# Optimization experiments

Measured on AMD Instinct MI355X. Metric: run time of the kernel, lower is better.

Reference implementation:

```python
import jax, jax.numpy as jnp
import numpy as np

HEADS = 4
DIM_HEAD = 32
GROUPS = 32  # min(256//4, 32)
EPS = 1e-5


def setup_inputs() -> dict:
    key = jax.random.key(0)
    ks = jax.random.split(key, 5)
    B, C, H, W = 16, 256, 64, 64
    CD, HC, WC = 512, 32, 32
    hid = HEADS * DIM_HEAD  # 128
    return {
        "x": jax.random.normal(ks[0], (B, C, H, W), jnp.float32),
        "cond": jax.random.normal(ks[1], (B, CD, HC, WC), jnp.float32),
        "gn_w": jnp.ones((C,), jnp.float32),
        "gn_b": jnp.zeros((C,), jnp.float32),
        "w_q": jax.random.normal(ks[2], (hid, C), jnp.float32) * 0.05,
        "b_q": jnp.zeros((hid,), jnp.float32),
        "w_kv": jax.random.normal(ks[3], (2 * hid, CD), jnp.float32) * 0.05,
        "b_kv": jnp.zeros((2 * hid,), jnp.float32),
        "w_out": jax.random.normal(ks[4], (C, hid), jnp.float32) * 0.05,
        "b_out": jnp.zeros((C,), jnp.float32),
    }


def _group_norm(x, w, b):
    # x: (B, C, H, W); normalize per group over (channels-in-group, H, W)
    B, C, H, W = x.shape
    xg = x.reshape(B, GROUPS, C // GROUPS, H, W)
    mu = jnp.mean(xg, axis=(2, 3, 4), keepdims=True)
    var = jnp.var(xg, axis=(2, 3, 4), keepdims=True)
    xn = ((xg - mu) * jax.lax.rsqrt(var + EPS)).reshape(B, C, H, W)
    return xn * w[None, :, None, None] + b[None, :, None, None]


def _conv1x1(x, w, b):
    # x: (B, Cin, H, W), w: (Cout, Cin), b: (Cout,)
    return jnp.einsum('oc,bchw->bohw', w, x) + b[None, :, None, None]


def reference(x, cond, gn_w, gn_b, w_q, b_q, w_kv, b_kv, w_out, b_out):
    B, C, H, W = x.shape
    hid = HEADS * DIM_HEAD
    xn = _group_norm(x, gn_w, gn_b)
    q = _conv1x1(xn, w_q, b_q)          # (B, hid, H, W)
    kv = _conv1x1(cond, w_kv, b_kv)     # (B, 2*hid, Hc, Wc)
    Nc = kv.shape[2] * kv.shape[3]
    N = H * W
    k = kv[:, :hid].reshape(B, HEADS, DIM_HEAD, Nc)
    v = kv[:, hid:].reshape(B, HEADS, DIM_HEAD, Nc)
    q = q.reshape(B, HEADS, DIM_HEAD, N)
    k = jax.nn.softmax(k, axis=-1)
    # kv outer product: (B, heads, d, e)
    context = jnp.einsum('bhdn,bhen->bhde', k, v)
    # query contraction over d: (B, heads, e, n)
    out = jnp.einsum('bhde,bhdn->bhen', context, q)
    out = out.reshape(B, hid, H, W)
    return _conv1x1(out, w_out, b_out)
```

## Files before the change

### kernel.cpp

```cpp
#include <hip/hip_runtime.h>
#include <hip/hip_bf16.h>

typedef __attribute__((ext_vector_type(8))) short bf16x8;
typedef __attribute__((ext_vector_type(4))) float f32x4;

__device__ __forceinline__ ushort f2bf(float f) {
    __hip_bfloat16 h = __float2bfloat16(f);
    return __builtin_bit_cast(ushort, h);
}
__device__ __forceinline__ unsigned pack2(float a, float b) {
    return (unsigned)f2bf(a) | ((unsigned)f2bf(b) << 16);
}
__device__ __forceinline__ float bflo(unsigned u) { return __uint_as_float(u << 16); }
__device__ __forceinline__ float bfhi(unsigned u) { return __uint_as_float(u & 0xffff0000u); }

__device__ __forceinline__ void unpack8(uint4 r, float* o) {
    o[0] = bflo(r.x); o[1] = bfhi(r.x); o[2] = bflo(r.y); o[3] = bfhi(r.y);
    o[4] = bflo(r.z); o[5] = bfhi(r.z); o[6] = bflo(r.w); o[7] = bfhi(r.w);
}

__global__ __launch_bounds__(256) void kv_gemm(const float* __restrict__ w_kv,
                                               const float* __restrict__ cond,
                                               const float* __restrict__ b_kv,
                                               ushort* __restrict__ kv16,
                                               float* __restrict__ zbase) {
    __shared__ ushort lA[128 * 64];
    __shared__ ushort lB[32 * 64];
    __shared__ float scratch[64 * 32];
    int nc = blockIdx.x, rb = blockIdx.y, b = blockIdx.z;
    int t = threadIdx.x;
    int fid = blockIdx.x + 32 * (blockIdx.y + 2 * blockIdx.z);
    if (fid < 264) zbase[fid * 256 + t] = 0.f;
    int col0 = nc * 32, row0 = rb * 128;
    int l = t & 63, w = t >> 6;
    int lr = l & 15, lg = l >> 4;
    const float* Ab32 = w_kv + (size_t)row0 * 512;
    const float* Bb = cond + (size_t)b * 512 * 1024 + col0;
    int rA = t >> 3, gAr = t & 7, gw = gAr ^ (rA & 7);
    int rB = t >> 3, gB = t & 7;
    int sp = t & 31, sj4 = (t >> 5) & 7;
    float4 ka0_, ka1_, ka2_, ka3_, ka4_, ka5_, ka6_, ka7_;
    float4 kb0_, kb1_;
#define KG_LOADA(k0) { \
    ka0_ = *(const float4*)&Ab32[(size_t)(rA)      * 512 + (k0) + gAr * 8]; \
    ka1_ = *(const float4*)&Ab32[(size_t)(rA)      * 512 + (k0) + gAr * 8 + 4]; \
    ka2_ = *(const float4*)&Ab32[(size_t)(32 + rA) * 512 + (k0) + gAr * 8]; \
    ka3_ = *(const float4*)&Ab32[(size_t)(32 + rA) * 512 + (k0) + gAr * 8 + 4]; \
    ka4_ = *(const float4*)&Ab32[(size_t)(64 + rA) * 512 + (k0) + gAr * 8]; \
    ka5_ = *(const float4*)&Ab32[(size_t)(64 + rA) * 512 + (k0) + gAr * 8 + 4]; \
    ka6_ = *(const float4*)&Ab32[(size_t)(96 + rA) * 512 + (k0) + gAr * 8]; \
    ka7_ = *(const float4*)&Ab32[(size_t)(96 + rA) * 512 + (k0) + gAr * 8 + 4]; }
#define KG_LOADB(k0) { \
    kb0_ = *(const float4*)&Bb[(size_t)((k0) + rB)      * 1024 + gB * 4]; \
    kb1_ = *(const float4*)&Bb[(size_t)((k0) + 32 + rB) * 1024 + gB * 4]; }
#define KG_WRITEA() { uint4 p; \
    p.x = pack2(ka0_.x, ka0_.y); p.y = pack2(ka0_.z, ka0_.w); \
    p.z = pack2(ka1_.x, ka1_.y); p.w = pack2(ka1_.z, ka1_.w); \
    *(uint4*)((char*)lA + (size_t)((rA)      * 8 + gw) * 16) = p; \
    p.x = pack2(ka2_.x, ka2_.y); p.y = pack2(ka2_.z, ka2_.w); \
    p.z = pack2(ka3_.x, ka3_.y); p.w = pack2(ka3_.z, ka3_.w); \
    *(uint4*)((char*)lA + (size_t)((32 + rA) * 8 + gw) * 16) = p; \
    p.x = pack2(ka4_.x, ka4_.y); p.y = pack2(ka4_.z, ka4_.w); \
    p.z = pack2(ka5_.x, ka5_.y); p.w = pack2(ka5_.z, ka5_.w); \
    *(uint4*)((char*)lA + (size_t)((64 + rA) * 8 + gw) * 16) = p; \
    p.x = pack2(ka6_.x, ka6_.y); p.y = pack2(ka6_.z, ka6_.w); \
    p.z = pack2(ka7_.x, ka7_.y); p.w = pack2(ka7_.z, ka7_.w); \
    *(uint4*)((char*)lA + (size_t)((96 + rA) * 8 + gw) * 16) = p; }
#define KG_WRITEB() { \
    *(float4*)((char*)scratch + (rB)      * 128 + ((gB ^ (((rB)      >> 1) & 7)) * 16)) = kb0_; \
    *(float4*)((char*)scratch + (32 + rB) * 128 + ((gB ^ (((32 + rB) >> 1) & 7)) * 16)) = kb1_; }
#define KG_PACKB() { \
    int js = sj4 ^ (sp & 7); \
    float4 s0 = *(const float4*)((char*)scratch + (2*sp)   * 128 + js * 16); \
    float4 s2 = *(const float4*)((char*)scratch + (2*sp+1) * 128 + js * 16); \
    float c0v[4] = {s0.x, s0.y, s0.z, s0.w}; \
    float c1v[4] = {s2.x, s2.y, s2.z, s2.w}; \
    _Pragma("unroll") \
    for (int w4 = 0; w4 < 4; ++w4) { \
        int n = sj4 * 4 + w4; \
        unsigned pk = pack2(c0v[w4], c1v[w4]); \
        *(unsigned*)((char*)lB + n * 128 + (((sp >> 2) ^ (n & 7)) * 16) + (sp & 3) * 4) = pk; \
    } }
    KG_LOADA(0); KG_LOADB(0);
    f32x4 acc[2][2] = {};
    for (int it = 0; it < 8; ++it) {
        KG_WRITEA();
        KG_WRITEB();
        __syncthreads();
        if (it < 7) { KG_LOADA(it * 64 + 64); KG_LOADB(it * 64 + 64); }
        KG_PACKB();
        __syncthreads();
        __builtin_amdgcn_s_setprio(1);
        #pragma unroll
        for (int ks = 0; ks < 2; ++ks) {
            bf16x8 av[2], bv[2];
            #pragma unroll
            for (int mi = 0; mi < 2; ++mi) {
                int ar = w * 32 + mi * 16 + lr;
                int q = (ks * 4 + lg) ^ (ar & 7);
                av[mi] = *(const bf16x8*)((const char*)lA + ar * 128 + q * 16);
            }
            #pragma unroll
            for (int ni = 0; ni < 2; ++ni) {
                int br = ni * 16 + lr;
                int q = (ks * 4 + lg) ^ (br & 7);
                bv[ni] = *(const bf16x8*)((const char*)lB + br * 128 + q * 16);
            }
            #pragma unroll
            for (int mi = 0; mi < 2; ++mi)
                #pragma unroll
                for (int ni = 0; ni < 2; ++ni)
                    acc[mi][ni] = __builtin_amdgcn_mfma_f32_16x16x32_bf16(
                        av[mi], bv[ni], acc[mi][ni], 0, 0, 0);
        }
        __builtin_amdgcn_s_setprio(0);
        __syncthreads();
    }
#undef KG_LOADA
#undef KG_LOADB
#undef KG_WRITEA
#undef KG_WRITEB
#undef KG_PACKB
    int orow = row0 + w * 32;
    #pragma unroll
    for (int mi = 0; mi < 2; ++mi) {
        int rbase = orow + mi * 16 + lg * 4;
        float4 b4 = *(const float4*)&b_kv[rbase];
        float bvr[4] = {b4.x, b4.y, b4.z, b4.w};
        #pragma unroll
        for (int ni = 0; ni < 2; ++ni) {
            int cc = col0 + ni * 16 + lr;
            #pragma unroll
            for (int r = 0; r < 4; ++r)
                kv16[((size_t)b * 256 + rbase + r) * 1024 + cc] = f2bf(acc[mi][ni][r] + bvr[r]);
        }
    }
}

__global__ __launch_bounds__(256) void ctxstats_kernel(const ushort* __restrict__ kv,
                                                       const float* __restrict__ x,
                                                       float* __restrict__ rowsum,
                                                       float* __restrict__ ctx,
                                                       float* __restrict__ statacc) {
    __shared__ float pl[32][129], vl[32][129];
    int bid = blockIdx.x, t = threadIdx.x;
    if (bid < 512) {
        int bh = bid >> 3, b = bh >> 2, h = bh & 3;
        int n0 = (bid & 7) * 128;
        int r = t >> 3, cs = (t & 7) * 16;
        const ushort* kp = kv + ((size_t)b * 256 + h * 32 + r) * 1024 + n0 + cs;
        const ushort* vp = kv + ((size_t)b * 256 + 128 + h * 32 + r) * 1024 + n0 + cs;
        float kvals[16], vvals[16];
        unpack8(((const uint4*)kp)[0], kvals);
        unpack8(((const uint4*)kp)[1], kvals + 8);
        unpack8(((const uint4*)vp)[0], vvals);
        unpack8(((const uint4*)vp)[1], vvals + 8);
        float psum = 0.f;
        #pragma unroll
        for (int i = 0; i < 16; ++i) {
            float e = __expf(kvals[i]);
            pl[r][cs + i] = e;
            vl[r][cs + i] = vvals[i];
            psum += e;
        }
        psum += __shfl_xor(psum, 1, 64);
        psum += __shfl_xor(psum, 2, 64);
        psum += __shfl_xor(psum, 4, 64);
        if ((t & 7) == 0) atomicAdd(&rowsum[bh * 32 + r], psum);
        __syncthreads();
        int d0 = t >> 5, e0 = t & 31;
        float acc[4] = {0.f, 0.f, 0.f, 0.f};
        #pragma unroll 8
        for (int nn = 0; nn < 128; ++nn) {
            float vv = vl[e0][nn];
            #pragma unroll
            for (int i = 0; i < 4; ++i)
                acc[i] += pl[d0 + 8 * i][nn] * vv;
        }
        #pragma unroll
        for (int i = 0; i < 4; ++i)
            atomicAdd(&ctx[((size_t)bh * 32 + d0 + 8 * i) * 32 + e0], acc[i]);
    } else {
        int bg = bid - 512;
        const float4* xp = (const float4*)(x + (size_t)bg * 32768);
        float s = 0.f, ss = 0.f;
        #pragma unroll
        for (int j = 0; j < 32; ++j) {
            float4 v = xp[t + 256 * j];
            s  += v.x + v.y + v.z + v.w;
            ss += v.x*v.x + v.y*v.y + v.z*v.z + v.w*v.w;
        }
        #pragma unroll
        for (int off = 32; off > 0; off >>= 1) {
            s  += __shfl_down(s, off, 64);
            ss += __shfl_down(ss, off, 64);
        }
        int wave = t >> 6;
        if ((t & 63) == 0) { pl[0][wave * 2] = s; pl[0][wave * 2 + 1] = ss; }
        __syncthreads();
        if (t == 0) {
            statacc[bg * 2]     = pl[0][0] + pl[0][2] + pl[0][4] + pl[0][6];
            statacc[bg * 2 + 1] = pl[0][1] + pl[0][3] + pl[0][5] + pl[0][7];
        }
    }
}

__global__ __launch_bounds__(256) void a_kernel(const float* __restrict__ ctx,
                                                const float* __restrict__ rowsum,
                                                const float* __restrict__ w_out,
                                                const float* __restrict__ w_q,
                                                const float* __restrict__ b_q,
                                                const float* __restrict__ b_out,
                                                ushort* __restrict__ A16,
                                                float* __restrict__ biasb) {
    __shared__ float ctxl[4][32][33];
    __shared__ float wol[16][128];
    __shared__ float ml[16][128];
    int b = blockIdx.x >> 4, ot = (blockIdx.x & 15) << 4;
    int t = threadIdx.x;
    #pragma unroll
    for (int j = 0; j < 16; ++j) {
        int e = t + 256 * j;
        float inv = 1.f / rowsum[b * 128 + (e >> 5)];
        ctxl[e >> 10][(e >> 5) & 31][e & 31] = ctx[(size_t)b * 4096 + e] * inv;
    }
    #pragma unroll
    for (int j = 0; j < 8; ++j) {
        int e = t + 256 * j;
        wol[e >> 7][e & 127] = w_out[(ot + (e >> 7)) * 128 + (e & 127)];
    }
    __syncthreads();
    #pragma unroll
    for (int j = 0; j < 8; ++j) {
        int e = t + 256 * j;
        int o = e >> 7, hd = e & 127, h = hd >> 5, d = hd & 31;
        float acc = 0.f;
        #pragma unroll
        for (int ee = 0; ee < 32; ++ee) acc += wol[o][h * 32 + ee] * ctxl[h][d][ee];
        ml[o][hd] = acc;
    }
    __syncthreads();
    int c = t;
    float wt[16];
    #pragma unroll
    for (int o = 0; o < 16; ++o) wt[o] = 0.f;
    for (int hd = 0; hd < 128; ++hd) {
        float wq = w_q[hd * 256 + c];
        #pragma unroll
        for (int o = 0; o < 16; ++o) wt[o] += ml[o][hd] * wq;
    }
    ushort* Abp = A16 + ((size_t)b * 256 + ot) * 256 + c;
    #pragma unroll
    for (int o = 0; o < 16; ++o)
        Abp[(size_t)o * 256] = f2bf(wt[o]);
    if (t < 16) {
        int o = t;
        float md = 0.f;
        #pragma unroll 8
        for (int hd = 0; hd < 128; ++hd) md += ml[o][hd] * b_q[hd];
        biasb[(size_t)b * 256 + ot + o] = md + b_out[ot + o];
    }
}

__global__ __launch_bounds__(512) void out_gemm_fused(const ushort* __restrict__ A16,
                                                      const float* __restrict__ x,
                                                      const float* __restrict__ statacc,
                                                      const float* __restrict__ gn_w,
                                                      const float* __restrict__ gn_b,
                                                      const float* __restrict__ biasb,
                                                      float* __restrict__ out) {
    __shared__ ushort lA[256 * 64];
    __shared__ ushort lB[64 * 64];
    __shared__ float scratch[64 * 64];
    __shared__ float sct[256][2];
    int b = blockIdx.y;
    int n0 = blockIdx.x * 64;
    int t = threadIdx.x;
    int l = t & 63, wid = t >> 6;
    int wr = wid >> 1, wc = wid & 1;
    int lr = l & 15, lg = l >> 4;
    const ushort* Ab = A16 + (size_t)b * 65536;
    const float* xb = x + (size_t)b * 256 * 4096 + n0;
    int sp = t & 31, sj4 = t >> 5;
    if (t < 256) {
        int g = t >> 3;
        float S  = statacc[(b * 32 + g) * 2];
        float SS = statacc[(b * 32 + g) * 2 + 1];
        float mu  = S * (1.f / 32768.f);
        float var = SS * (1.f / 32768.f) - mu * mu;
        float sc = rsqrtf(var + 1e-5f) * gn_w[t];
        sct[t][0] = sc;
        sct[t][1] = gn_b[t] - mu * sc;
    }
    uint4 a0_, a1_, a2_, a3_;
    float4 b0_, b1_;
    float4 c0_, c1_;
    int rA = t >> 3, gA = (t & 7) ^ (rA & 7);
    int rB = t >> 4, gB = t & 15;
#define OG_LOADA(k0) { \
    a0_ = *(const uint4*)(Ab + (size_t)(rA)       * 256 + (k0) + gA * 8); \
    a1_ = *(const uint4*)(Ab + (size_t)(64 + rA)  * 256 + (k0) + gA * 8); \
    a2_ = *(const uint4*)(Ab + (size_t)(128 + rA) * 256 + (k0) + gA * 8); \
    a3_ = *(const uint4*)(Ab + (size_t)(192 + rA) * 256 + (k0) + gA * 8); }
#define OG_LOADB0(k0) { \
    b0_ = *(const float4*)&xb[(size_t)((k0) + rB)      * 4096 + gB * 4]; \
    b1_ = *(const float4*)&xb[(size_t)((k0) + 32 + rB) * 4096 + gB * 4]; }
#define OG_LOADB1(k0) { \
    c0_ = *(const float4*)&xb[(size_t)((k0) + rB)      * 4096 + gB * 4]; \
    c1_ = *(const float4*)&xb[(size_t)((k0) + 32 + rB) * 4096 + gB * 4]; }
#define OG_WRITEB(v0, v1) { \
    *(float4*)((char*)scratch + (rB)      * 256 + ((gB ^ (((rB)      >> 1) & 15)) * 16)) = v0; \
    *(float4*)((char*)scratch + (32 + rB) * 256 + ((gB ^ (((32 + rB) >> 1) & 15)) * 16)) = v1; }
    OG_LOADA(0); OG_LOADB0(0); 
    f32x4 acc[4][2] = {};
    for (int it = 0; it < 4; ++it) {
        int k0 = it * 64;
        *(uint4*)((char*)lA + (size_t)t * 16)          = a0_;
        *(uint4*)((char*)lA + (size_t)(512 + t) * 16)  = a1_;
        *(uint4*)((char*)lA + (size_t)(1024 + t) * 16) = a2_;
        *(uint4*)((char*)lA + (size_t)(1536 + t) * 16) = a3_;
        if (it & 1) { OG_WRITEB(c0_, c1_); } else { OG_WRITEB(b0_, b1_); }
        __syncthreads();
        if (it < 3) OG_LOADA(k0 + 64);
        if (it == 0) OG_LOADB1(64);
        if (it == 1 && 1) OG_LOADB0(128);
        if (it == 2) OG_LOADB1(192);
        {
            int js = sj4 ^ (sp & 15);
            float sc0 = sct[k0 + 2 * sp][0],     tc0 = sct[k0 + 2 * sp][1];
            float sc1 = sct[k0 + 2 * sp + 1][0], tc1 = sct[k0 + 2 * sp + 1][1];
            float4 s0 = *(const float4*)((char*)scratch + (2*sp)   * 256 + js * 16);
            float4 s2 = *(const float4*)((char*)scratch + (2*sp+1) * 256 + js * 16);
            float c0v[4] = {s0.x, s0.y, s0.z, s0.w};
            float c1v[4] = {s2.x, s2.y, s2.z, s2.w};
            #pragma unroll
            for (int w4 = 0; w4 < 4; ++w4) {
                int n = sj4 * 4 + w4;
                unsigned pk = pack2(c0v[w4] * sc0 + tc0, c1v[w4] * sc1 + tc1);
                *(unsigned*)((char*)lB + n * 128 + (((sp >> 2) ^ (n & 7)) * 16) + (sp & 3) * 4) = pk;
            }
        }
        __syncthreads();
        __builtin_amdgcn_s_setprio(1);
        #pragma unroll
        for (int ks = 0; ks < 2; ++ks) {
            bf16x8 av[4], bv[2];
            #pragma unroll
            for (int mi = 0; mi < 4; ++mi) {
                int ar = wr * 64 + mi * 16 + lr;
                int q = (ks * 4 + lg) ^ (ar & 7);
                av[mi] = *(const bf16x8*)((const char*)lA + ar * 128 + q * 16);
            }
            #pragma unroll
            for (int ni = 0; ni < 2; ++ni) {
                int br = wc * 32 + ni * 16 + lr;
                int q = (ks * 4 + lg) ^ (br & 7);
                bv[ni] = *(const bf16x8*)((const char*)lB + br * 128 + q * 16);
            }
            #pragma unroll
            for (int mi = 0; mi < 4; ++mi)
                #pragma unroll
                for (int ni = 0; ni < 2; ++ni)
                    acc[mi][ni] = __builtin_amdgcn_mfma_f32_16x16x32_bf16(
                        av[mi], bv[ni], acc[mi][ni], 0, 0, 0);
        }
        __builtin_amdgcn_s_setprio(0);
        __syncthreads();
    }
#undef OG_LOADA
#undef OG_LOADB0
#undef OG_LOADB1
#undef OG_WRITEB
    const float* bp = biasb + (size_t)b * 256;
    int orow = wr * 64, ocol = n0 + wc * 32 + lr;
    #pragma unroll
    for (int mi = 0; mi < 4; ++mi) {
        int rb2 = orow + mi * 16 + lg * 4;
        float4 b4 = *(const float4*)&bp[rb2];
        float bvr[4] = {b4.x, b4.y, b4.z, b4.w};
        #pragma unroll
        for (int ni = 0; ni < 2; ++ni) {
            int cc = ocol + ni * 16;
            #pragma unroll
            for (int r = 0; r < 4; ++r)
                out[((size_t)b * 256 + rb2 + r) * 4096 + cc] = acc[mi][ni][r] + bvr[r];
        }
    }
}

extern "C" void kernel_launch(void* const* d_in, const int* in_sizes, int n_in,
                              void* d_out, int out_size, void* d_ws, size_t ws_size,
                              hipStream_t stream) {
    const float* x     = (const float*)d_in[0];
    const float* cond  = (const float*)d_in[1];
    const float* gn_w  = (const float*)d_in[2];
    const float* gn_b  = (const float*)d_in[3];
    const float* w_q   = (const float*)d_in[4];
    const float* b_q   = (const float*)d_in[5];
    const float* w_kv  = (const float*)d_in[6];
    const float* b_kv  = (const float*)d_in[7];
    const float* w_out = (const float*)d_in[8];
    const float* b_out = (const float*)d_in[9];
    float* out = (float*)d_out;

    float* f       = (float*)d_ws;
    float* statacc = f;
    float* rowsum  = f + 1024;
    float* ctx     = f + 3072;
    float* biasb   = f + 68608;
    ushort* u      = (ushort*)(f + 72704);
    ushort* kv16   = u;
    ushort* A16    = u + 4194304;

    kv_gemm<<<dim3(32, 2, 16), 256, 0, stream>>>(w_kv, cond, b_kv, kv16, rowsum);
    ctxstats_kernel<<<1024, 256, 0, stream>>>(kv16, x, rowsum, ctx, statacc);
    a_kernel<<<256, 256, 0, stream>>>(ctx, rowsum, w_out, w_q, b_q, b_out, A16, biasb);
    out_gemm_fused<<<dim3(64, 16), 512, 0, stream>>>(A16, x, statacc, gn_w, gn_b, biasb, out);
}
```

Before: 78.29 us.

## Fold GroupNorm affine into A16 weights and bias; swizzle block order for XCD locality

```diff
diff --git a/kernel.cpp b/kernel.cpp
--- a/kernel.cpp
+++ b/kernel.cpp
@@ -27,10 +27,12 @@
     __shared__ ushort lA[128 * 64];
     __shared__ ushort lB[32 * 64];
     __shared__ float scratch[64 * 32];
-    int nc = blockIdx.x, rb = blockIdx.y, b = blockIdx.z;
+    int bid0 = blockIdx.x;
+    int swz = (bid0 & 7) * 128 + (bid0 >> 3);
+    int b = swz >> 6, rem = swz & 63;
+    int rb = rem >> 5, nc = rem & 31;
     int t = threadIdx.x;
-    int fid = blockIdx.x + 32 * (blockIdx.y + 2 * blockIdx.z);
-    if (fid < 264) zbase[fid * 256 + t] = 0.f;
+    if (bid0 < 264) zbase[bid0 * 256 + t] = 0.f;
     int col0 = nc * 32, row0 = rb * 128;
     int l = t & 63, w = t >> 6;
     int lr = l & 15, lg = l >> 4;
@@ -210,12 +212,17 @@
                                                 const float* __restrict__ w_out,
                                                 const float* __restrict__ w_q,
                                                 const float* __restrict__ b_q,
+                                                const float* __restrict__ statacc,
+                                                const float* __restrict__ gn_w,
+                                                const float* __restrict__ gn_b,
                                                 const float* __restrict__ b_out,
                                                 ushort* __restrict__ A16,
                                                 float* __restrict__ biasb) {
     __shared__ float ctxl[4][32][33];
     __shared__ float wol[16][128];
     __shared__ float ml[16][128];
+    __shared__ float cbuf[256][17];
+    __shared__ float pbuf[16][17];
     int b = blockIdx.x >> 4, ot = (blockIdx.x & 15) << 4;
     int t = threadIdx.x;
     #pragma unroll
@@ -240,7 +247,12 @@
         ml[o][hd] = acc;
     }
     __syncthreads();
-    int c = t;
+    int c = t, g = c >> 3;
+    float a0 = statacc[(b * 32 + g) * 2], a1 = statacc[(b * 32 + g) * 2 + 1];
+    float mu  = a0 * (1.f / 32768.f);
+    float var = a1 * (1.f / 32768.f) - mu * mu;
+    float sc = rsqrtf(var + 1e-5f) * gn_w[c];
+    float tc = gn_b[c] - mu * sc;
     float wt[16];
     #pragma unroll
     for (int o = 0; o < 16; ++o) wt[o] = 0.f;
@@ -251,30 +263,42 @@
     }
     ushort* Abp = A16 + ((size_t)b * 256 + ot) * 256 + c;
     #pragma unroll
-    for (int o = 0; o < 16; ++o)
-        Abp[(size_t)o * 256] = f2bf(wt[o]);
+    for (int o = 0; o < 16; ++o) {
+        Abp[(size_t)o * 256] = f2bf(wt[o] * sc);
+        cbuf[c][o] = wt[o] * tc;
+    }
+    __syncthreads();
+    {
+        int o = t >> 4, seg = t & 15;
+        float p = 0.f;
+        #pragma unroll
+        for (int i = 0; i < 16; ++i) p += cbuf[seg * 16 + i][o];
+        pbuf[o][seg] = p;
+    }
+    __syncthreads();
     if (t < 16) {
         int o = t;
+        float sum = 0.f;
+        #pragma unroll
+        for (int s2 = 0; s2 < 16; ++s2) sum += pbuf[o][s2];
         float md = 0.f;
         #pragma unroll 8
         for (int hd = 0; hd < 128; ++hd) md += ml[o][hd] * b_q[hd];
-        biasb[(size_t)b * 256 + ot + o] = md + b_out[ot + o];
+        biasb[(size_t)b * 256 + ot + o] = sum + md + b_out[ot + o];
     }
 }
 
 __global__ __launch_bounds__(512) void out_gemm_fused(const ushort* __restrict__ A16,
                                                       const float* __restrict__ x,
-                                                      const float* __restrict__ statacc,
-                                                      const float* __restrict__ gn_w,
-                                                      const float* __restrict__ gn_b,
                                                       const float* __restrict__ biasb,
                                                       float* __restrict__ out) {
     __shared__ ushort lA[256 * 64];
     __shared__ ushort lB[64 * 64];
     __shared__ float scratch[64 * 64];
-    __shared__ float sct[256][2];
-    int b = blockIdx.y;
-    int n0 = blockIdx.x * 64;
+    int bid0 = blockIdx.x;
+    int swz = (bid0 & 7) * 128 + (bid0 >> 3);
+    int b = swz >> 6, nb = swz & 63;
+    int n0 = nb * 64;
     int t = threadIdx.x;
     int l = t & 63, wid = t >> 6;
     int wr = wid >> 1, wc = wid & 1;
@@ -282,16 +306,6 @@
     const ushort* Ab = A16 + (size_t)b * 65536;
     const float* xb = x + (size_t)b * 256 * 4096 + n0;
     int sp = t & 31, sj4 = t >> 5;
-    if (t < 256) {
-        int g = t >> 3;
-        float S  = statacc[(b * 32 + g) * 2];
-        float SS = statacc[(b * 32 + g) * 2 + 1];
-        float mu  = S * (1.f / 32768.f);
-        float var = SS * (1.f / 32768.f) - mu * mu;
-        float sc = rsqrtf(var + 1e-5f) * gn_w[t];
-        sct[t][0] = sc;
-        sct[t][1] = gn_b[t] - mu * sc;
-    }
     uint4 a0_, a1_, a2_, a3_;
     float4 b0_, b1_;
     float4 c0_, c1_;
@@ -311,7 +325,7 @@
 #define OG_WRITEB(v0, v1) { \
     *(float4*)((char*)scratch + (rB)      * 256 + ((gB ^ (((rB)      >> 1) & 15)) * 16)) = v0; \
     *(float4*)((char*)scratch + (32 + rB) * 256 + ((gB ^ (((32 + rB) >> 1) & 15)) * 16)) = v1; }
-    OG_LOADA(0); OG_LOADB0(0); 
+    OG_LOADA(0); OG_LOADB0(0);
     f32x4 acc[4][2] = {};
     for (int it = 0; it < 4; ++it) {
         int k0 = it * 64;
@@ -323,12 +337,10 @@
         __syncthreads();
         if (it < 3) OG_LOADA(k0 + 64);
         if (it == 0) OG_LOADB1(64);
-        if (it == 1 && 1) OG_LOADB0(128);
+        if (it == 1) OG_LOADB0(128);
         if (it == 2) OG_LOADB1(192);
         {
             int js = sj4 ^ (sp & 15);
-            float sc0 = sct[k0 + 2 * sp][0],     tc0 = sct[k0 + 2 * sp][1];
-            float sc1 = sct[k0 + 2 * sp + 1][0], tc1 = sct[k0 + 2 * sp + 1][1];
             float4 s0 = *(const float4*)((char*)scratch + (2*sp)   * 256 + js * 16);
             float4 s2 = *(const float4*)((char*)scratch + (2*sp+1) * 256 + js * 16);
             float c0v[4] = {s0.x, s0.y, s0.z, s0.w};
@@ -336,7 +348,7 @@
             #pragma unroll
             for (int w4 = 0; w4 < 4; ++w4) {
                 int n = sj4 * 4 + w4;
-                unsigned pk = pack2(c0v[w4] * sc0 + tc0, c1v[w4] * sc1 + tc1);
+                unsigned pk = pack2(c0v[w4], c1v[w4]);
                 *(unsigned*)((char*)lB + n * 128 + (((sp >> 2) ^ (n & 7)) * 16) + (sp & 3) * 4) = pk;
             }
         }
@@ -412,8 +424,9 @@
     ushort* kv16   = u;
     ushort* A16    = u + 4194304;
 
-    kv_gemm<<<dim3(32, 2, 16), 256, 0, stream>>>(w_kv, cond, b_kv, kv16, rowsum);
+    kv_gemm<<<1024, 256, 0, stream>>>(w_kv, cond, b_kv, kv16, rowsum);
     ctxstats_kernel<<<1024, 256, 0, stream>>>(kv16, x, rowsum, ctx, statacc);
-    a_kernel<<<256, 256, 0, stream>>>(ctx, rowsum, w_out, w_q, b_q, b_out, A16, biasb);
-    out_gemm_fused<<<dim3(64, 16), 512, 0, stream>>>(A16, x, statacc, gn_w, gn_b, biasb, out);
-}
+    a_kernel<<<256, 256, 0, stream>>>(ctx, rowsum, w_out, w_q, b_q, statacc,
+                                      gn_w, gn_b, b_out, A16, biasb);
+    out_gemm_fused<<<1024, 512, 0, stream>>>(A16, x, biasb, out);
+}
```

New measurement: 82.30 us. 1.05x slower.
